# Kernel tuning notes

Measured on AMD Instinct MI355X. Metric: run time of the kernel, lower is better.

The kernel has to match this reference:

```python
import jax, jax.numpy as jnp
import numpy as np

DIM = 2048
N_HEADS = 16
HEAD_DIM = DIM // N_HEADS  # 128
MAX_LEN = 2048
B, T = 2, 2048
RESTORE_SCALE = DIM ** 0.5  # sqkinit / sqkscale = 1 / (1/sqrt(dim))
SQK_SCALE = 1.0 / DIM ** 0.5


def _rope_tables(seq_len, head_dim, dtype=jnp.float32):
    d2 = head_dim // 2
    pos = jnp.arange(seq_len, dtype=dtype)                     # [T]
    theta = 1.0 / (10000.0 ** (jnp.arange(0, head_dim, 2, dtype=dtype) / head_dim))  # [d2]
    ang = pos[:, None] * theta[None, :]                        # [T, d2]
    return jnp.cos(ang), jnp.sin(ang)


def _apply_rope(x, cos, sin):
    # x: [B, H, T, D]; cos/sin: [T, D/2] broadcast over B,H
    d2 = x.shape[-1] // 2
    xr, xi = x[..., :d2], x[..., d2:]
    return jnp.concatenate([xr * cos - xi * sin, xr * sin + xi * cos], axis=-1)


def setup_inputs() -> dict:
    key = jax.random.key(0)
    ks = jax.random.split(key, 5)
    s = 0.02
    return {
        "x":  jax.random.normal(ks[0], (B, T, DIM), jnp.float32),
        "Wq": jax.random.normal(ks[1], (DIM, DIM), jnp.float32) * s,
        "Wk": jax.random.normal(ks[2], (DIM, DIM), jnp.float32) * s,
        "Wv": jax.random.normal(ks[3], (DIM, DIM), jnp.float32) * s,
        "Wo": jax.random.normal(ks[4], (DIM, DIM), jnp.float32) * s,
        "sqk": jnp.ones((N_HEADS, 1, HEAD_DIM), jnp.float32) * SQK_SCALE,
    }


def reference(x, Wq, Wk, Wv, Wo, sqk):
    Bc, Tc, C = x.shape
    # QKV projections (torch Linear: x @ W.T), split heads -> [B, H, T, D]
    def proj(W):
        return (x @ W.T).reshape(Bc, Tc, N_HEADS, HEAD_DIM).transpose(0, 2, 1, 3)
    q, k, v = proj(Wq), proj(Wk), proj(Wv)

    cos, sin = _rope_tables(Tc, HEAD_DIM, x.dtype)
    actual_sqk = sqk * RESTORE_SCALE  # [H, 1, D]
    q = _apply_rope(q, cos, sin) * actual_sqk
    k = _apply_rope(k, cos, sin) * actual_sqk

    # SDPA with scale = sqrt(head_dim) (as in the source, not 1/sqrt)
    scale = HEAD_DIM ** 0.5
    scores = jnp.einsum("bhtd,bhsd->bhts", q, k) * scale  # [B, H, T, T]
    causal = jnp.tril(jnp.ones((Tc, Tc), bool))
    scores = jnp.where(causal, scores, -jnp.inf)
    attn = jax.nn.softmax(scores, axis=-1)
    out = jnp.einsum("bhts,bhsd->bhtd", attn, v)           # [B, H, T, D]
    out = out.transpose(0, 2, 1, 3).reshape(Bc, Tc, C)

    y = out @ Wo.T
    # F.normalize(p=2, dim=-1, eps=1e-12)
    norm = jnp.linalg.norm(y, axis=-1, keepdims=True)
    return y / jnp.maximum(norm, 1e-12)
```

## Files before the change

kernel.cpp:

```cpp
#include <hip/hip_runtime.h>

#define DEVFN __device__ __forceinline__

typedef float    floatx4 __attribute__((ext_vector_type(4)));
typedef _Float16 half8   __attribute__((ext_vector_type(8)));
typedef _Float16 half4v  __attribute__((ext_vector_type(4)));

#define MFMA16H(a, b, c) __builtin_amdgcn_mfma_f32_16x16x32_f16((a), (b), (c), 0, 0, 0)

DEVFN void async16(void* lds, const void* g) {
  __builtin_amdgcn_global_load_lds(
      (const __attribute__((address_space(1))) unsigned int*)g,
      (__attribute__((address_space(3))) unsigned int*)lds, 16, 0, 0);
}
DEVFN half8 ld8h(const _Float16* p) { return *(const half8*)p; }

__global__ __launch_bounds__(256) void cvt_prep(
    const float4* __restrict__ x, const float4* __restrict__ wq,
    const float4* __restrict__ wk, const float4* __restrict__ wv,
    const float4* __restrict__ wo,
    half4v* __restrict__ xh, half4v* __restrict__ xl,
    half4v* __restrict__ qo, half4v* __restrict__ ko,
    half4v* __restrict__ vo, half4v* __restrict__ oo,
    float* __restrict__ cosT, float* __restrict__ sinT) {
  int i = blockIdx.x * 256 + threadIdx.x;
  {
    float4 v = x[i];
    half4v h = {(_Float16)v.x, (_Float16)v.y, (_Float16)v.z, (_Float16)v.w};
    half4v l = {(_Float16)(v.x - (float)h.x), (_Float16)(v.y - (float)h.y),
                (_Float16)(v.z - (float)h.z), (_Float16)(v.w - (float)h.w)};
    xh[i] = h;
    xl[i] = l;
  }
  if (i < 1048576) {
    float4 v = wq[i];
    qo[i] = (half4v){(_Float16)v.x, (_Float16)v.y, (_Float16)v.z, (_Float16)v.w};
    v = wk[i];
    ko[i] = (half4v){(_Float16)v.x, (_Float16)v.y, (_Float16)v.z, (_Float16)v.w};
    v = wv[i];
    vo[i] = (half4v){(_Float16)v.x, (_Float16)v.y, (_Float16)v.z, (_Float16)v.w};
    v = wo[i];
    oo[i] = (half4v){(_Float16)v.x, (_Float16)v.y, (_Float16)v.z, (_Float16)v.w};
  }
  if (i < 131072) {
    int t = i >> 6, d = i & 63;
    double theta = exp(-((double)(2 * d) / 128.0) * log(10000.0));
    double ang = (double)t * theta;
    cosT[i] = (float)cos(ang);
    sinT[i] = (float)sin(ang);
  }
}

__global__ __launch_bounds__(512, 2) void gemm_qk_f16(
    const _Float16* __restrict__ xhp, const _Float16* __restrict__ xlp,
    const _Float16* __restrict__ wqp, const _Float16* __restrict__ wkp,
    const float* __restrict__ cosT, const float* __restrict__ sinT,
    const float* __restrict__ sqk,
    _Float16* __restrict__ qhi, _Float16* __restrict__ qlo,
    _Float16* __restrict__ khi) {
  constexpr int Kd = 2048, NT = 64;
  const int n0 = blockIdx.x * 128, m0 = blockIdx.y * 256;
  const int tid = threadIdx.x, w = tid >> 6, lane = tid & 63;
  const int quad = lane >> 4, l16 = lane & 15;
  const int c0 = w & 1, rb = w >> 1, rgb = rb * 4;
  const int cgr0 = 2 * c0, cgr1 = 2 * c0 + 1, cgr2 = 2 * c0 + 4, cgr3 = 2 * c0 + 5;

  __shared__ __align__(16) _Float16 smem[57344];
  _Float16* XH = smem;
  _Float16* XL = smem + 16384;
  _Float16* WQ = smem + 32768;
  _Float16* WK = smem + 45056;

  floatx4 accQ[4][4], accK[4][4];
#pragma unroll
  for (int i = 0; i < 4; i++)
#pragma unroll
    for (int c = 0; c < 4; c++) {
      accQ[i][c] = (floatx4){0.f, 0.f, 0.f, 0.f};
      accK[i][c] = (floatx4){0.f, 0.f, 0.f, 0.f};
    }

  const size_t xg0 = (size_t)(m0 + 32 * w + l16) * Kd + quad * 8;
  const size_t xg1 = xg0 + (size_t)16 * Kd;
  const size_t wg = (size_t)(n0 + 16 * w + l16) * Kd + quad * 8;

#define STAGE_X(T)                                                      \
  {                                                                     \
    const int kk_ = (T) * 32;                                           \
    _Float16* bx_ = XH + ((T) & 1) * 8192;                              \
    _Float16* bl_ = XL + ((T) & 1) * 8192;                              \
    async16(bx_ + (2 * w) * 512, xhp + xg0 + kk_);                      \
    async16(bx_ + (2 * w + 1) * 512, xhp + xg1 + kk_);                  \
    async16(bl_ + (2 * w) * 512, xlp + xg0 + kk_);                      \
    async16(bl_ + (2 * w + 1) * 512, xlp + xg1 + kk_);                  \
  }
#define STAGE_W(T)                                                      \
  {                                                                     \
    const int kk_ = (T) * 32;                                           \
    async16(WQ + ((T) % 3) * 4096 + w * 512, wqp + wg + kk_);           \
    async16(WK + ((T) % 3) * 4096 + w * 512, wkp + wg + kk_);           \
  }

  STAGE_X(0);
  STAGE_W(0);
  STAGE_W(1);
  asm volatile("s_waitcnt vmcnt(2)" ::: "memory");
  __builtin_amdgcn_s_barrier();

#pragma unroll 1
  for (int t = 0; t < NT; ++t) {
    const _Float16* XH_ = XH + (t & 1) * 8192;
    const _Float16* XL_ = XL + (t & 1) * 8192;
    const _Float16* WQ_ = WQ + (t % 3) * 4096;
    const _Float16* WK_ = WK + (t % 3) * 4096;

    half8 ah[4], al[4], bq[4];
#pragma unroll
    for (int i = 0; i < 4; i++) {
      ah[i] = ld8h(XH_ + (rgb + i) * 512 + lane * 8);
      al[i] = ld8h(XL_ + (rgb + i) * 512 + lane * 8);
    }
    bq[0] = ld8h(WQ_ + cgr0 * 512 + lane * 8);
    bq[1] = ld8h(WQ_ + cgr1 * 512 + lane * 8);
    bq[2] = ld8h(WQ_ + cgr2 * 512 + lane * 8);
    bq[3] = ld8h(WQ_ + cgr3 * 512 + lane * 8);
    if (t + 1 < NT) STAGE_X(t + 1);
    __builtin_amdgcn_s_barrier();
    asm volatile("s_waitcnt lgkmcnt(0)");
    __builtin_amdgcn_sched_barrier(0);
    __builtin_amdgcn_s_setprio(1);
#pragma unroll
    for (int i = 0; i < 4; i++)
#pragma unroll
      for (int c = 0; c < 4; c++)
        accQ[i][c] = MFMA16H(ah[i], bq[c], accQ[i][c]);
#pragma unroll
    for (int i = 0; i < 4; i++)
#pragma unroll
      for (int c = 0; c < 4; c++)
        accQ[i][c] = MFMA16H(al[i], bq[c], accQ[i][c]);
    __builtin_amdgcn_s_setprio(0);
    __builtin_amdgcn_s_barrier();

    half8 bk[4];
    bk[0] = ld8h(WK_ + cgr0 * 512 + lane * 8);
    bk[1] = ld8h(WK_ + cgr1 * 512 + lane * 8);
    bk[2] = ld8h(WK_ + cgr2 * 512 + lane * 8);
    bk[3] = ld8h(WK_ + cgr3 * 512 + lane * 8);
    if (t + 2 < NT) STAGE_W(t + 2);
    __builtin_amdgcn_s_barrier();
    asm volatile("s_waitcnt lgkmcnt(0)");
    __builtin_amdgcn_sched_barrier(0);
    __builtin_amdgcn_s_setprio(1);
#pragma unroll
    for (int i = 0; i < 4; i++)
#pragma unroll
      for (int c = 0; c < 4; c++)
        accK[i][c] = MFMA16H(ah[i], bk[c], accK[i][c]);
#pragma unroll
    for (int i = 0; i < 4; i++)
#pragma unroll
      for (int c = 0; c < 4; c++)
        accK[i][c] = MFMA16H(al[i], bk[c], accK[i][c]);
    __builtin_amdgcn_s_setprio(0);

    if (t + 2 < NT) {
      asm volatile("s_waitcnt vmcnt(2)" ::: "memory");
    } else {
      asm volatile("s_waitcnt vmcnt(0)" ::: "memory");
    }
    __builtin_amdgcn_s_barrier();
  }
#undef STAGE_X
#undef STAGE_W

  _Float16* stH = smem + w * 1152;
  _Float16* stL = smem + 9216 + w * 1152;

  const int h = n0 >> 7;
  const int b = m0 >> 11;

#pragma unroll
  for (int rg = 0; rg < 4; rg++) {
    const int tt0 = (m0 & 2047) + rb * 64 + rg * 16;
    const size_t gbase = (((size_t)(b * 16 + h)) * 2048 + tt0) * 128;

#pragma unroll
    for (int cj = 0; cj < 2; cj++) {
      int d = c0 * 32 + cj * 16 + l16;
      float s1 = sqk[h * 128 + d] * 512.0f;
      float s2 = sqk[h * 128 + d + 64] * 512.0f;
#pragma unroll
      for (int r = 0; r < 4; r++) {
        int tq = tt0 + quad * 4 + r;
        float cc = cosT[tq * 64 + d], sn = sinT[tq * 64 + d];
        float xr = accQ[rg][cj][r], xi = accQ[rg][cj + 2][r];
        float o1 = (xr * cc - xi * sn) * s1;
        float o2 = (xr * sn + xi * cc) * s2;
        _Float16 h1 = (_Float16)o1, h2 = (_Float16)o2;
        int rl = quad * 4 + r;
        stH[rl * 72 + cj * 16 + l16] = h1;
        stH[rl * 72 + 32 + cj * 16 + l16] = h2;
        stL[rl * 72 + cj * 16 + l16] = (_Float16)(o1 - (float)h1);
        stL[rl * 72 + 32 + cj * 16 + l16] = (_Float16)(o2 - (float)h2);
      }
    }
#pragma unroll
    for (int it = 0; it < 2; it++) {
      int row = it * 8 + (lane >> 3), pc = (lane & 7) * 8;
      int d = (pc < 32) ? (c0 * 32 + pc) : (64 + c0 * 32 + (pc - 32));
      size_t ga = gbase + (size_t)row * 128 + d;
      *(half8*)(qhi + ga) = ld8h(&stH[row * 72 + pc]);
      *(half8*)(qlo + ga) = ld8h(&stL[row * 72 + pc]);
    }

#pragma unroll
    for (int cj = 0; cj < 2; cj++) {
      int d = c0 * 32 + cj * 16 + l16;
      float s1 = sqk[h * 128 + d] * 45.254834f;
      float s2 = sqk[h * 128 + d + 64] * 45.254834f;
#pragma unroll
      for (int r = 0; r < 4; r++) {
        int tq = tt0 + quad * 4 + r;
        float cc = cosT[tq * 64 + d], sn = sinT[tq * 64 + d];
        float xr = accK[rg][cj][r], xi = accK[rg][cj + 2][r];
        int rl = quad * 4 + r;
        stH[rl * 72 + cj * 16 + l16] = (_Float16)((xr * cc - xi * sn) * s1);
        stH[rl * 72 + 32 + cj * 16 + l16] = (_Float16)((xr * sn + xi * cc) * s2);
      }
    }
#pragma unroll
    for (int it = 0; it < 2; it++) {
      int row = it * 8 + (lane >> 3), pc = (lane & 7) * 8;
      int d = (pc < 32) ? (c0 * 32 + pc) : (64 + c0 * 32 + (pc - 32));
      *(half8*)(khi + gbase + (size_t)row * 128 + d) = ld8h(&stH[row * 72 + pc]);
    }
  }
}

__global__ __launch_bounds__(512, 2) void gemm_v_f16(
    const _Float16* __restrict__ xhp, const _Float16* __restrict__ wvp,
    _Float16* __restrict__ vt) {
  constexpr int Kd = 2048, NT = 64;
  const int n0 = blockIdx.x * 128, m0 = blockIdx.y * 256;
  const int tid = threadIdx.x, w = tid >> 6, lane = tid & 63;
  const int quad = lane >> 4, l16 = lane & 15;
  const int c0 = w & 1, rb = w >> 1, rgb = rb * 4;

  __shared__ __align__(16) _Float16 smem[28672];
  _Float16* XH = smem;
  _Float16* WV = smem + 16384;

  floatx4 accV[4][4];
#pragma unroll
  for (int i = 0; i < 4; i++)
#pragma unroll
    for (int c = 0; c < 4; c++) accV[i][c] = (floatx4){0.f, 0.f, 0.f, 0.f};

  const size_t xg0 = (size_t)(m0 + 32 * w + l16) * Kd + quad * 8;
  const size_t xg1 = xg0 + (size_t)16 * Kd;
  const size_t wg = (size_t)(n0 + 16 * w + l16) * Kd + quad * 8;

#define STAGE_XV(T)                                                     \
  {                                                                     \
    const int kk_ = (T) * 32;                                           \
    _Float16* bx_ = XH + ((T) & 1) * 8192;                              \
    async16(bx_ + (2 * w) * 512, xhp + xg0 + kk_);                      \
    async16(bx_ + (2 * w + 1) * 512, xhp + xg1 + kk_);                  \
  }
#define STAGE_WV(T)                                                     \
  { async16(WV + ((T) % 3) * 4096 + w * 512, wvp + wg + (T) * 32); }

  STAGE_XV(0);
  STAGE_WV(0);
  STAGE_WV(1);
  asm volatile("s_waitcnt vmcnt(1)" ::: "memory");
  __builtin_amdgcn_s_barrier();

#pragma unroll 1
  for (int t = 0; t < NT; ++t) {
    const _Float16* XH_ = XH + (t & 1) * 8192;
    const _Float16* WV_ = WV + (t % 3) * 4096;

    half8 ah[4], bv[4];
#pragma unroll
    for (int i = 0; i < 4; i++)
      ah[i] = ld8h(XH_ + (rgb + i) * 512 + lane * 8);
#pragma unroll
    for (int c = 0; c < 4; c++)
      bv[c] = ld8h(WV_ + (4 * c0 + c) * 512 + lane * 8);
    if (t + 1 < NT) STAGE_XV(t + 1);
    if (t + 2 < NT) STAGE_WV(t + 2);
    __builtin_amdgcn_s_barrier();
    asm volatile("s_waitcnt lgkmcnt(0)");
    __builtin_amdgcn_sched_barrier(0);
    __builtin_amdgcn_s_setprio(1);
#pragma unroll
    for (int i = 0; i < 4; i++)
#pragma unroll
      for (int c = 0; c < 4; c++)
        accV[i][c] = MFMA16H(ah[i], bv[c], accV[i][c]);
    __builtin_amdgcn_s_setprio(0);
    if (t + 2 < NT) {
      asm volatile("s_waitcnt vmcnt(1)" ::: "memory");
    } else {
      asm volatile("s_waitcnt vmcnt(0)" ::: "memory");
    }
    __builtin_amdgcn_s_barrier();
  }
#undef STAGE_XV
#undef STAGE_WV

  _Float16* stV = smem + w * 1024;

  const int h = n0 >> 7;
  const int b = m0 >> 11;
  const int bh = b * 16 + h;

#pragma unroll
  for (int rg = 0; rg < 4; rg++) {
    const int tt0 = (m0 & 2047) + rb * 64 + rg * 16;
#pragma unroll
    for (int c = 0; c < 4; c++)
#pragma unroll
      for (int r = 0; r < 4; r++)
        stV[(c * 16 + l16) * 16 + quad * 4 + r] = (_Float16)accV[rg][c][r];
#pragma unroll
    for (int it = 0; it < 2; it++) {
      int dl = it * 32 + (lane >> 1), th = (lane & 1) * 8;
      int dh = c0 * 64 + dl;
      size_t ga = ((size_t)bh * 128 + dh) * 2048 + tt0 + th;
      *(half8*)(vt + ga) = ld8h(&stV[dl * 16 + th]);
    }
  }
}

__global__ __launch_bounds__(256, 2) void flash_attn(
    const _Float16* __restrict__ qhp, const _Float16* __restrict__ qlp,
    const _Float16* __restrict__ khp,
    const _Float16* __restrict__ vtp, _Float16* __restrict__ aout) {
  constexpr int T = 2048, HD = 128;
  const int bh = blockIdx.x, qt = blockIdx.y;
  const int q0 = qt * 128;
  const int tid = threadIdx.x, w = tid >> 6, lane = tid & 63;
  const int quad = lane >> 4, l16 = lane & 15;

  __shared__ __align__(16) _Float16 Kh[2][8192];
  __shared__ __align__(16) _Float16 Vt[2][8192];
  __shared__ __align__(16) _Float16 Pb[4][16 * 72];

  const size_t qkbase = (size_t)bh * T * HD;

  half8 qh[2][4], ql[2][4];
#pragma unroll
  for (int i = 0; i < 2; i++)
#pragma unroll
    for (int s = 0; s < 4; s++) {
      size_t off = qkbase + (size_t)(q0 + w * 32 + i * 16 + l16) * HD + s * 32 + quad * 8;
      qh[i][s] = *(const half8*)(qhp + off);
      ql[i][s] = *(const half8*)(qlp + off);
    }

  floatx4 o[2][8];
#pragma unroll
  for (int i = 0; i < 2; i++)
#pragma unroll
    for (int dt = 0; dt < 8; dt++) o[i][dt] = (floatx4){0.f, 0.f, 0.f, 0.f};
  float mrow[2][4], lrow[2][4];
#pragma unroll
  for (int i = 0; i < 2; i++)
#pragma unroll
    for (int r = 0; r < 4; r++) { mrow[i][r] = -3e38f; lrow[i][r] = 0.f; }

  const int ntiles = q0 / 64 + 2;

  auto stageKV = [&](int kt, int set) {
    const int s0 = kt * 64;
    for (int c = w; c < 16; c += 4) {
      int tt = c >> 2, ss = c & 3;
      size_t go = qkbase + (size_t)(s0 + tt * 16 + l16) * HD + ss * 32 + quad * 8;
      async16(&Kh[set][c * 512], khp + go);
      int dt = c >> 1, vs = c & 1;
      size_t vo = (size_t)bh * HD * T + (size_t)(dt * 16 + l16) * T + s0 + vs * 32 + quad * 8;
      async16(&Vt[set][c * 512], vtp + vo);
    }
  };

  stageKV(0, 0);
  __syncthreads();

  for (int kt = 0; kt < ntiles; ++kt) {
    const int s0 = kt * 64;
    const int set = kt & 1;
    if (kt + 1 < ntiles) stageKV(kt + 1, set ^ 1);

    floatx4 S[2][4];
#pragma unroll
    for (int i = 0; i < 2; i++)
#pragma unroll
      for (int j = 0; j < 4; j++) S[i][j] = (floatx4){0.f, 0.f, 0.f, 0.f};

#pragma unroll
    for (int s = 0; s < 4; s++) {
#pragma unroll
      for (int j = 0; j < 4; j++) {
        half8 kh = ld8h(&Kh[set][(j * 4 + s) * 512 + lane * 8]);
        S[0][j] = MFMA16H(qh[0][s], kh, S[0][j]);
        S[1][j] = MFMA16H(qh[1][s], kh, S[1][j]);
        S[0][j] = MFMA16H(ql[0][s], kh, S[0][j]);
        S[1][j] = MFMA16H(ql[1][s], kh, S[1][j]);
      }
    }

    if (s0 + 63 > q0) {
#pragma unroll
      for (int i = 0; i < 2; i++) {
        int rb = q0 + w * 32 + i * 16 + quad * 4;
#pragma unroll
        for (int j = 0; j < 4; j++) {
          int cg = s0 + j * 16 + l16;
#pragma unroll
          for (int r = 0; r < 4; r++)
            if (cg > rb + r) S[i][j][r] = -3e38f;
        }
      }
    }

    half8 pf[2][2];
#pragma unroll
    for (int i = 0; i < 2; i++) {
#pragma unroll
      for (int r = 0; r < 4; r++) {
        float mx = fmaxf(fmaxf(S[i][0][r], S[i][1][r]), fmaxf(S[i][2][r], S[i][3][r]));
#pragma unroll
        for (int d = 1; d < 16; d <<= 1) mx = fmaxf(mx, __shfl_xor(mx, d, 64));
        float mnew = fmaxf(mrow[i][r], mx);
        float al = __expf(mrow[i][r] - mnew);
        mrow[i][r] = mnew;
        float sum = 0.f;
#pragma unroll
        for (int j = 0; j < 4; j++) {
          float p = __expf(S[i][j][r] - mnew);
          S[i][j][r] = p;
          sum += p;
        }
#pragma unroll
        for (int d = 1; d < 16; d <<= 1) sum += __shfl_xor(sum, d, 64);
        lrow[i][r] = lrow[i][r] * al + sum;
#pragma unroll
        for (int dt = 0; dt < 8; dt++) o[i][dt][r] *= al;
      }
#pragma unroll
      for (int r = 0; r < 4; r++)
#pragma unroll
        for (int j = 0; j < 4; j++)
          Pb[w][(quad * 4 + r) * 72 + j * 16 + l16] = (_Float16)S[i][j][r];
      pf[i][0] = ld8h(&Pb[w][l16 * 72 + quad * 8]);
      pf[i][1] = ld8h(&Pb[w][l16 * 72 + 32 + quad * 8]);
    }

#pragma unroll
    for (int dt = 0; dt < 8; dt++) {
#pragma unroll
      for (int s = 0; s < 2; s++) {
        half8 vf = ld8h(&Vt[set][(dt * 2 + s) * 512 + lane * 8]);
        o[0][dt] = MFMA16H(pf[0][s], vf, o[0][dt]);
        o[1][dt] = MFMA16H(pf[1][s], vf, o[1][dt]);
      }
    }
    __syncthreads();
  }

  const int b = bh >> 4, h = bh & 15;
#pragma unroll
  for (int i = 0; i < 2; i++) {
#pragma unroll
    for (int r = 0; r < 4; r++) {
      int trow = q0 + w * 32 + i * 16 + quad * 4 + r;
      float linv = 1.0f / lrow[i][r];
      size_t base = ((size_t)(b * T + trow)) * 2048 + h * 128;
#pragma unroll
      for (int dt = 0; dt < 8; dt++)
        aout[base + dt * 16 + l16] = (_Float16)(o[i][dt][r] * linv);
    }
  }
}

__global__ __launch_bounds__(256, 2) void gemm_o_f16(
    const _Float16* __restrict__ A, const _Float16* __restrict__ B,
    float* __restrict__ outF) {
  constexpr int Kd = 2048;
  constexpr int Nd = 2048;
  const int n0 = blockIdx.x * 128, m0 = blockIdx.y * 128;
  const int tid = threadIdx.x, w = tid >> 6, lane = tid & 63;
  const int quad = lane >> 4, l16 = lane & 15;

  __shared__ __align__(16) _Float16 As[8192];
  __shared__ __align__(16) _Float16 Bs[8192];

  floatx4 acc[2][8];
#pragma unroll
  for (int i = 0; i < 2; i++)
#pragma unroll
    for (int j = 0; j < 8; j++) acc[i][j] = (floatx4){0.f, 0.f, 0.f, 0.f};

  const int t0 = 2 * w, t1 = 2 * w + 1;
  const size_t ao0 = (size_t)(m0 + t0 * 16 + l16) * Kd + quad * 8;
  const size_t ao1 = (size_t)(m0 + t1 * 16 + l16) * Kd + quad * 8;
  const size_t bo0 = (size_t)(n0 + t0 * 16 + l16) * Kd + quad * 8;
  const size_t bo1 = (size_t)(n0 + t1 * 16 + l16) * Kd + quad * 8;

  for (int k0 = 0; k0 < Kd; k0 += 64) {
    __syncthreads();
    async16(&As[t0 * 512], A + ao0 + k0);
    async16(&As[t1 * 512], A + ao1 + k0);
    async16(&As[4096 + t0 * 512], A + ao0 + k0 + 32);
    async16(&As[4096 + t1 * 512], A + ao1 + k0 + 32);
    async16(&Bs[t0 * 512], B + bo0 + k0);
    async16(&Bs[t1 * 512], B + bo1 + k0);
    async16(&Bs[4096 + t0 * 512], B + bo0 + k0 + 32);
    async16(&Bs[4096 + t1 * 512], B + bo1 + k0 + 32);
    __syncthreads();
    half8 a00 = ld8h(&As[t0 * 512 + lane * 8]);
    half8 a10 = ld8h(&As[t1 * 512 + lane * 8]);
    half8 a01 = ld8h(&As[4096 + t0 * 512 + lane * 8]);
    half8 a11 = ld8h(&As[4096 + t1 * 512 + lane * 8]);
#pragma unroll
    for (int j = 0; j < 8; j++) {
      half8 b0 = ld8h(&Bs[j * 512 + lane * 8]);
      acc[0][j] = MFMA16H(a00, b0, acc[0][j]);
      acc[1][j] = MFMA16H(a10, b0, acc[1][j]);
      half8 b1 = ld8h(&Bs[4096 + j * 512 + lane * 8]);
      acc[0][j] = MFMA16H(a01, b1, acc[0][j]);
      acc[1][j] = MFMA16H(a11, b1, acc[1][j]);
    }
  }

#pragma unroll
  for (int i = 0; i < 2; i++) {
    int rbase = m0 + (2 * w + i) * 16 + quad * 4;
#pragma unroll
    for (int j = 0; j < 8; j++) {
      int col = n0 + j * 16 + l16;
#pragma unroll
      for (int r = 0; r < 4; r++)
        outF[(size_t)(rbase + r) * Nd + col] = acc[i][j][r];
    }
  }
}

__global__ __launch_bounds__(256) void rownorm(const float* __restrict__ y,
                                               float* __restrict__ out) {
  int row = blockIdx.x;
  const float4* yr = (const float4*)(y + (size_t)row * 2048);
  float4* od = (float4*)(out + (size_t)row * 2048);
  int t = threadIdx.x;
  float4 v0 = yr[t], v1 = yr[t + 256];
  float ss = v0.x * v0.x + v0.y * v0.y + v0.z * v0.z + v0.w * v0.w +
             v1.x * v1.x + v1.y * v1.y + v1.z * v1.z + v1.w * v1.w;
#pragma unroll
  for (int d = 1; d < 64; d <<= 1) ss += __shfl_xor(ss, d, 64);
  __shared__ float red[4];
  if ((t & 63) == 0) red[t >> 6] = ss;
  __syncthreads();
  float tot = red[0] + red[1] + red[2] + red[3];
  float inv = 1.0f / fmaxf(sqrtf(tot), 1e-12f);
  v0.x *= inv; v0.y *= inv; v0.z *= inv; v0.w *= inv;
  v1.x *= inv; v1.y *= inv; v1.z *= inv; v1.w *= inv;
  od[t] = v0;
  od[t + 256] = v1;
}

extern "C" void kernel_launch(void* const* d_in, const int* in_sizes, int n_in,
                              void* d_out, int out_size, void* d_ws, size_t ws_size,
                              hipStream_t stream) {
  (void)in_sizes; (void)n_in; (void)out_size; (void)ws_size;
  const float* x   = (const float*)d_in[0];
  const float* Wq  = (const float*)d_in[1];
  const float* Wk  = (const float*)d_in[2];
  const float* Wv  = (const float*)d_in[3];
  const float* Wo  = (const float*)d_in[4];
  const float* sqk = (const float*)d_in[5];
  char* ws = (char*)d_ws;

  constexpr size_t SZX = 8388608ull * 2;
  constexpr size_t SZW = 4194304ull * 2;

  size_t o_xh = 0;
  size_t o_xl = o_xh + SZX;
  size_t o_wq = o_xl + SZX;
  size_t o_wk = o_wq + SZW;
  size_t o_wv = o_wk + SZW;
  size_t o_wo = o_wv + SZW;
  size_t o_qh = o_wo + SZW;
  size_t o_ql = o_qh + SZX;
  size_t o_kh = o_ql + SZX;
  size_t o_v  = o_kh + SZX;
  size_t o_vt = o_v + SZX;
  size_t o_cos = o_vt + SZX;
  size_t o_sin = o_cos + 2048 * 64 * 4;
  size_t o_aout = o_wq;
  size_t o_y    = o_qh;

  _Float16* xh = (_Float16*)(ws + o_xh);
  _Float16* xl = (_Float16*)(ws + o_xl);
  _Float16* wq = (_Float16*)(ws + o_wq);
  _Float16* wk = (_Float16*)(ws + o_wk);
  _Float16* wv = (_Float16*)(ws + o_wv);
  _Float16* wo = (_Float16*)(ws + o_wo);
  _Float16* qh = (_Float16*)(ws + o_qh);
  _Float16* ql = (_Float16*)(ws + o_ql);
  _Float16* kh = (_Float16*)(ws + o_kh);
  _Float16* vt = (_Float16*)(ws + o_vt);
  float* cosT = (float*)(ws + o_cos);
  float* sinT = (float*)(ws + o_sin);
  _Float16* aout = (_Float16*)(ws + o_aout);
  float* y = (float*)(ws + o_y);

  cvt_prep<<<8192, 256, 0, stream>>>((const float4*)x, (const float4*)Wq,
                                     (const float4*)Wk, (const float4*)Wv,
                                     (const float4*)Wo, (half4v*)xh, (half4v*)xl,
                                     (half4v*)wq, (half4v*)wk, (half4v*)wv,
                                     (half4v*)wo, cosT, sinT);

  gemm_qk_f16<<<dim3(16, 16), 512, 0, stream>>>(xh, xl, wq, wk, cosT, sinT,
                                                sqk, qh, ql, kh);
  gemm_v_f16<<<dim3(16, 16), 512, 0, stream>>>(xh, wv, vt);

  flash_attn<<<dim3(32, 16), 256, 0, stream>>>(qh, ql, kh, vt, aout);

  gemm_o_f16<<<dim3(16, 32), 256, 0, stream>>>(aout, wo, y);
  rownorm<<<4096, 256, 0, stream>>>(y, (float*)d_out);
}
```

Baseline: 534.3 us.

## Pair causal query tiles per block, add lazy max rescale and MFMA priority

Each flash-attention block now handles two query tiles, p and 15-p, so every block does the same amount of causal work. This halves the grid and removes the load-imbalance tail. The online softmax only rescales the accumulator when some row's new max exceeds the running max by more than 8, which skips most rescales and batches the shuffle reductions across rows. The MFMA sections are wrapped in s_setprio to favour matrix issue; the risks are less parallelism across the grid and larger unnormalized exponents, up to e^8, in fp16 P.

```diff
diff --git a/kernel.cpp b/kernel.cpp
--- a/kernel.cpp
+++ b/kernel.cpp
@@ -340,8 +340,7 @@
     const _Float16* __restrict__ khp,
     const _Float16* __restrict__ vtp, _Float16* __restrict__ aout) {
   constexpr int T = 2048, HD = 128;
-  const int bh = blockIdx.x, qt = blockIdx.y;
-  const int q0 = qt * 128;
+  const int bh = blockIdx.x, p = blockIdx.y;
   const int tid = threadIdx.x, w = tid >> 6, lane = tid & 63;
   const int quad = lane >> 4, l16 = lane & 15;
 
@@ -350,29 +349,7 @@
   __shared__ __align__(16) _Float16 Pb[4][16 * 72];
 
   const size_t qkbase = (size_t)bh * T * HD;
-
-  half8 qh[2][4], ql[2][4];
-#pragma unroll
-  for (int i = 0; i < 2; i++)
-#pragma unroll
-    for (int s = 0; s < 4; s++) {
-      size_t off = qkbase + (size_t)(q0 + w * 32 + i * 16 + l16) * HD + s * 32 + quad * 8;
-      qh[i][s] = *(const half8*)(qhp + off);
-      ql[i][s] = *(const half8*)(qlp + off);
-    }
-
-  floatx4 o[2][8];
-#pragma unroll
-  for (int i = 0; i < 2; i++)
-#pragma unroll
-    for (int dt = 0; dt < 8; dt++) o[i][dt] = (floatx4){0.f, 0.f, 0.f, 0.f};
-  float mrow[2][4], lrow[2][4];
-#pragma unroll
-  for (int i = 0; i < 2; i++)
-#pragma unroll
-    for (int r = 0; r < 4; r++) { mrow[i][r] = -3e38f; lrow[i][r] = 0.f; }
-
-  const int ntiles = q0 / 64 + 2;
+  const size_t vbase = (size_t)bh * HD * T;
 
   auto stageKV = [&](int kt, int set) {
     const int s0 = kt * 64;
@@ -381,107 +358,180 @@
       size_t go = qkbase + (size_t)(s0 + tt * 16 + l16) * HD + ss * 32 + quad * 8;
       async16(&Kh[set][c * 512], khp + go);
       int dt = c >> 1, vs = c & 1;
-      size_t vo = (size_t)bh * HD * T + (size_t)(dt * 16 + l16) * T + s0 + vs * 32 + quad * 8;
+      size_t vo = vbase + (size_t)(dt * 16 + l16) * T + s0 + vs * 32 + quad * 8;
       async16(&Vt[set][c * 512], vtp + vo);
     }
   };
 
-  stageKV(0, 0);
-  __syncthreads();
-
-  for (int kt = 0; kt < ntiles; ++kt) {
-    const int s0 = kt * 64;
-    const int set = kt & 1;
-    if (kt + 1 < ntiles) stageKV(kt + 1, set ^ 1);
-
-    floatx4 S[2][4];
+#pragma unroll 1
+  for (int half = 0; half < 2; ++half) {
+    const int qt = half ? (15 - p) : p;
+    const int q0 = qt * 128;
+
+    half8 qh[2][4], ql[2][4];
 #pragma unroll
     for (int i = 0; i < 2; i++)
 #pragma unroll
-      for (int j = 0; j < 4; j++) S[i][j] = (floatx4){0.f, 0.f, 0.f, 0.f};
-
-#pragma unroll
-    for (int s = 0; s < 4; s++) {
-#pragma unroll
-      for (int j = 0; j < 4; j++) {
-        half8 kh = ld8h(&Kh[set][(j * 4 + s) * 512 + lane * 8]);
-        S[0][j] = MFMA16H(qh[0][s], kh, S[0][j]);
-        S[1][j] = MFMA16H(qh[1][s], kh, S[1][j]);
-        S[0][j] = MFMA16H(ql[0][s], kh, S[0][j]);
-        S[1][j] = MFMA16H(ql[1][s], kh, S[1][j]);
-      }
-    }
-
-    if (s0 + 63 > q0) {
+      for (int s = 0; s < 4; s++) {
+        size_t off = qkbase + (size_t)(q0 + w * 32 + i * 16 + l16) * HD + s * 32 + quad * 8;
+        qh[i][s] = *(const half8*)(qhp + off);
+        ql[i][s] = *(const half8*)(qlp + off);
+      }
+
+    floatx4 o[2][8];
+#pragma unroll
+    for (int i = 0; i < 2; i++)
+#pragma unroll
+      for (int dt = 0; dt < 8; dt++) o[i][dt] = (floatx4){0.f, 0.f, 0.f, 0.f};
+    float mrow[2][4], lrow[2][4];
+#pragma unroll
+    for (int i = 0; i < 2; i++)
+#pragma unroll
+      for (int r = 0; r < 4; r++) { mrow[i][r] = -3e38f; lrow[i][r] = 0.f; }
+
+    const int ntiles = qt * 2 + 2;
+
+    stageKV(0, 0);
+    __syncthreads();
+
+#pragma unroll 1
+    for (int kt = 0; kt < ntiles; ++kt) {
+      const int s0 = kt * 64;
+      const int set = kt & 1;
+      if (kt + 1 < ntiles) stageKV(kt + 1, set ^ 1);
+
+      floatx4 S[2][4];
+#pragma unroll
+      for (int i = 0; i < 2; i++)
+#pragma unroll
+        for (int j = 0; j < 4; j++) S[i][j] = (floatx4){0.f, 0.f, 0.f, 0.f};
+
+      __builtin_amdgcn_s_setprio(1);
+#pragma unroll
+      for (int s = 0; s < 4; s++) {
+#pragma unroll
+        for (int j = 0; j < 4; j++) {
+          half8 kh = ld8h(&Kh[set][(j * 4 + s) * 512 + lane * 8]);
+          S[0][j] = MFMA16H(qh[0][s], kh, S[0][j]);
+          S[1][j] = MFMA16H(qh[1][s], kh, S[1][j]);
+          S[0][j] = MFMA16H(ql[0][s], kh, S[0][j]);
+          S[1][j] = MFMA16H(ql[1][s], kh, S[1][j]);
+        }
+      }
+      __builtin_amdgcn_s_setprio(0);
+
+      if (s0 + 63 > q0) {
+#pragma unroll
+        for (int i = 0; i < 2; i++) {
+          int rb = q0 + w * 32 + i * 16 + quad * 4;
+#pragma unroll
+          for (int j = 0; j < 4; j++) {
+            int cg = s0 + j * 16 + l16;
+#pragma unroll
+            for (int r = 0; r < 4; r++)
+              if (cg > rb + r) S[i][j][r] = -3e38f;
+          }
+        }
+      }
+
+      float lm[2][4];
+#pragma unroll
+      for (int i = 0; i < 2; i++)
+#pragma unroll
+        for (int r = 0; r < 4; r++)
+          lm[i][r] = fmaxf(fmaxf(S[i][0][r], S[i][1][r]),
+                           fmaxf(S[i][2][r], S[i][3][r]));
+
+      bool ok = true;
+#pragma unroll
+      for (int i = 0; i < 2; i++)
+#pragma unroll
+        for (int r = 0; r < 4; r++)
+          ok = ok && (lm[i][r] <= mrow[i][r] + 8.0f);
+
+      if (!__all(ok ? 1 : 0)) {
+#pragma unroll
+        for (int d = 1; d < 16; d <<= 1)
+#pragma unroll
+          for (int i = 0; i < 2; i++)
+#pragma unroll
+            for (int r = 0; r < 4; r++)
+              lm[i][r] = fmaxf(lm[i][r], __shfl_xor(lm[i][r], d, 64));
+#pragma unroll
+        for (int i = 0; i < 2; i++)
+#pragma unroll
+          for (int r = 0; r < 4; r++) {
+            float mnew = fmaxf(mrow[i][r], lm[i][r]);
+            float al = __expf(mrow[i][r] - mnew);
+            mrow[i][r] = mnew;
+            lrow[i][r] *= al;
+#pragma unroll
+            for (int dt = 0; dt < 8; dt++) o[i][dt][r] *= al;
+          }
+      }
+
+      float rs[2][4];
+#pragma unroll
+      for (int i = 0; i < 2; i++)
+#pragma unroll
+        for (int r = 0; r < 4; r++) {
+          float e0 = __expf(S[i][0][r] - mrow[i][r]);
+          float e1 = __expf(S[i][1][r] - mrow[i][r]);
+          float e2 = __expf(S[i][2][r] - mrow[i][r]);
+          float e3 = __expf(S[i][3][r] - mrow[i][r]);
+          S[i][0][r] = e0; S[i][1][r] = e1; S[i][2][r] = e2; S[i][3][r] = e3;
+          rs[i][r] = (e0 + e1) + (e2 + e3);
+        }
+#pragma unroll
+      for (int d = 1; d < 16; d <<= 1)
+#pragma unroll
+        for (int i = 0; i < 2; i++)
+#pragma unroll
+          for (int r = 0; r < 4; r++)
+            rs[i][r] += __shfl_xor(rs[i][r], d, 64);
+#pragma unroll
+      for (int i = 0; i < 2; i++)
+#pragma unroll
+        for (int r = 0; r < 4; r++) lrow[i][r] += rs[i][r];
+
+      half8 pf[2][2];
 #pragma unroll
       for (int i = 0; i < 2; i++) {
-        int rb = q0 + w * 32 + i * 16 + quad * 4;
-#pragma unroll
-        for (int j = 0; j < 4; j++) {
-          int cg = s0 + j * 16 + l16;
-#pragma unroll
-          for (int r = 0; r < 4; r++)
-            if (cg > rb + r) S[i][j][r] = -3e38f;
+#pragma unroll
+        for (int r = 0; r < 4; r++)
+#pragma unroll
+          for (int j = 0; j < 4; j++)
+            Pb[w][(quad * 4 + r) * 72 + j * 16 + l16] = (_Float16)S[i][j][r];
+        pf[i][0] = ld8h(&Pb[w][l16 * 72 + quad * 8]);
+        pf[i][1] = ld8h(&Pb[w][l16 * 72 + 32 + quad * 8]);
+      }
+
+      __builtin_amdgcn_s_setprio(1);
+#pragma unroll
+      for (int dt = 0; dt < 8; dt++) {
+#pragma unroll
+        for (int s = 0; s < 2; s++) {
+          half8 vf = ld8h(&Vt[set][(dt * 2 + s) * 512 + lane * 8]);
+          o[0][dt] = MFMA16H(pf[0][s], vf, o[0][dt]);
+          o[1][dt] = MFMA16H(pf[1][s], vf, o[1][dt]);
         }
       }
-    }
-
-    half8 pf[2][2];
+      __builtin_amdgcn_s_setprio(0);
+      __syncthreads();
+    }
+
+    const int b = bh >> 4, h = bh & 15;
 #pragma unroll
     for (int i = 0; i < 2; i++) {
 #pragma unroll
       for (int r = 0; r < 4; r++) {
-        float mx = fmaxf(fmaxf(S[i][0][r], S[i][1][r]), fmaxf(S[i][2][r], S[i][3][r]));
-#pragma unroll
-        for (int d = 1; d < 16; d <<= 1) mx = fmaxf(mx, __shfl_xor(mx, d, 64));
-        float mnew = fmaxf(mrow[i][r], mx);
-        float al = __expf(mrow[i][r] - mnew);
-        mrow[i][r] = mnew;
-        float sum = 0.f;
-#pragma unroll
-        for (int j = 0; j < 4; j++) {
-          float p = __expf(S[i][j][r] - mnew);
-          S[i][j][r] = p;
-          sum += p;
-        }
-#pragma unroll
-        for (int d = 1; d < 16; d <<= 1) sum += __shfl_xor(sum, d, 64);
-        lrow[i][r] = lrow[i][r] * al + sum;
-#pragma unroll
-        for (int dt = 0; dt < 8; dt++) o[i][dt][r] *= al;
-      }
-#pragma unroll
-      for (int r = 0; r < 4; r++)
-#pragma unroll
-        for (int j = 0; j < 4; j++)
-          Pb[w][(quad * 4 + r) * 72 + j * 16 + l16] = (_Float16)S[i][j][r];
-      pf[i][0] = ld8h(&Pb[w][l16 * 72 + quad * 8]);
-      pf[i][1] = ld8h(&Pb[w][l16 * 72 + 32 + quad * 8]);
-    }
-
-#pragma unroll
-    for (int dt = 0; dt < 8; dt++) {
-#pragma unroll
-      for (int s = 0; s < 2; s++) {
-        half8 vf = ld8h(&Vt[set][(dt * 2 + s) * 512 + lane * 8]);
-        o[0][dt] = MFMA16H(pf[0][s], vf, o[0][dt]);
-        o[1][dt] = MFMA16H(pf[1][s], vf, o[1][dt]);
-      }
-    }
-    __syncthreads();
-  }
-
-  const int b = bh >> 4, h = bh & 15;
-#pragma unroll
-  for (int i = 0; i < 2; i++) {
-#pragma unroll
-    for (int r = 0; r < 4; r++) {
-      int trow = q0 + w * 32 + i * 16 + quad * 4 + r;
-      float linv = 1.0f / lrow[i][r];
-      size_t base = ((size_t)(b * T + trow)) * 2048 + h * 128;
-#pragma unroll
-      for (int dt = 0; dt < 8; dt++)
-        aout[base + dt * 16 + l16] = (_Float16)(o[i][dt][r] * linv);
+        int trow = q0 + w * 32 + i * 16 + quad * 4 + r;
+        float linv = 1.0f / lrow[i][r];
+        size_t base = ((size_t)(b * T + trow)) * 2048 + h * 128;
+#pragma unroll
+        for (int dt = 0; dt < 8; dt++)
+          aout[base + dt * 16 + l16] = (_Float16)(o[i][dt][r] * linv);
+      }
     }
   }
 }
@@ -627,7 +677,7 @@
                                                 sqk, qh, ql, kh);
   gemm_v_f16<<<dim3(16, 16), 512, 0, stream>>>(xh, wv, vt);
 
-  flash_attn<<<dim3(32, 16), 256, 0, stream>>>(qh, ql, kh, vt, aout);
+  flash_attn<<<dim3(32, 8), 256, 0, stream>>>(qh, ql, kh, vt, aout);
 
   gemm_o_f16<<<dim3(16, 32), 256, 0, stream>>>(aout, wo, y);
   rownorm<<<4096, 256, 0, stream>>>(y, (float*)d_out);
```

Measured after the change: 527.6 us. Within noise of the previous version (-1.3%).

## Halve flash-attention query tile, reverse tile order, add lazy rescale and setprio

Applied to the files above, without the earlier changes.

The flash attention kernel now gives each block 64 query rows instead of 128, so each wave owns 16 rows, and the grid doubles to 32x32. Query tiles are scheduled longest-first by reversing the block index. The online softmax skips the max reduction and rescale when every lane's new local max stays within 8 of the running max. MFMA sections are wrapped in s_setprio. The aim is better occupancy, load balance across causal tiles and less softmax overhead, at the cost of more K/V reloads per query row and larger unnormalised exponent ranges in fp16 P.

```diff
diff --git a/kernel.cpp b/kernel.cpp
--- a/kernel.cpp
+++ b/kernel.cpp
@@ -340,8 +340,9 @@
     const _Float16* __restrict__ khp,
     const _Float16* __restrict__ vtp, _Float16* __restrict__ aout) {
   constexpr int T = 2048, HD = 128;
-  const int bh = blockIdx.x, qt = blockIdx.y;
-  const int q0 = qt * 128;
+  const int bh = blockIdx.x;
+  const int qt = 31 - blockIdx.y;
+  const int q0 = qt * 64;
   const int tid = threadIdx.x, w = tid >> 6, lane = tid & 63;
   const int quad = lane >> 4, l16 = lane & 15;
 
@@ -350,29 +351,7 @@
   __shared__ __align__(16) _Float16 Pb[4][16 * 72];
 
   const size_t qkbase = (size_t)bh * T * HD;
-
-  half8 qh[2][4], ql[2][4];
-#pragma unroll
-  for (int i = 0; i < 2; i++)
-#pragma unroll
-    for (int s = 0; s < 4; s++) {
-      size_t off = qkbase + (size_t)(q0 + w * 32 + i * 16 + l16) * HD + s * 32 + quad * 8;
-      qh[i][s] = *(const half8*)(qhp + off);
-      ql[i][s] = *(const half8*)(qlp + off);
-    }
-
-  floatx4 o[2][8];
-#pragma unroll
-  for (int i = 0; i < 2; i++)
-#pragma unroll
-    for (int dt = 0; dt < 8; dt++) o[i][dt] = (floatx4){0.f, 0.f, 0.f, 0.f};
-  float mrow[2][4], lrow[2][4];
-#pragma unroll
-  for (int i = 0; i < 2; i++)
-#pragma unroll
-    for (int r = 0; r < 4; r++) { mrow[i][r] = -3e38f; lrow[i][r] = 0.f; }
-
-  const int ntiles = q0 / 64 + 2;
+  const size_t vbase = (size_t)bh * HD * T;
 
   auto stageKV = [&](int kt, int set) {
     const int s0 = kt * 64;
@@ -381,108 +360,138 @@
       size_t go = qkbase + (size_t)(s0 + tt * 16 + l16) * HD + ss * 32 + quad * 8;
       async16(&Kh[set][c * 512], khp + go);
       int dt = c >> 1, vs = c & 1;
-      size_t vo = (size_t)bh * HD * T + (size_t)(dt * 16 + l16) * T + s0 + vs * 32 + quad * 8;
+      size_t vo = vbase + (size_t)(dt * 16 + l16) * T + s0 + vs * 32 + quad * 8;
       async16(&Vt[set][c * 512], vtp + vo);
     }
   };
+
+  half8 qh[4], ql[4];
+#pragma unroll
+  for (int s = 0; s < 4; s++) {
+    size_t off = qkbase + (size_t)(q0 + w * 16 + l16) * HD + s * 32 + quad * 8;
+    qh[s] = *(const half8*)(qhp + off);
+    ql[s] = *(const half8*)(qlp + off);
+  }
+
+  floatx4 o[8];
+#pragma unroll
+  for (int dt = 0; dt < 8; dt++) o[dt] = (floatx4){0.f, 0.f, 0.f, 0.f};
+  float mrow[4], lrow[4];
+#pragma unroll
+  for (int r = 0; r < 4; r++) { mrow[r] = -3e38f; lrow[r] = 0.f; }
+
+  const int ntiles = qt + 1;
 
   stageKV(0, 0);
   __syncthreads();
 
+#pragma unroll 1
   for (int kt = 0; kt < ntiles; ++kt) {
     const int s0 = kt * 64;
     const int set = kt & 1;
     if (kt + 1 < ntiles) stageKV(kt + 1, set ^ 1);
 
-    floatx4 S[2][4];
-#pragma unroll
-    for (int i = 0; i < 2; i++)
-#pragma unroll
-      for (int j = 0; j < 4; j++) S[i][j] = (floatx4){0.f, 0.f, 0.f, 0.f};
-
+    floatx4 S[4];
+#pragma unroll
+    for (int j = 0; j < 4; j++) S[j] = (floatx4){0.f, 0.f, 0.f, 0.f};
+
+    __builtin_amdgcn_s_setprio(1);
 #pragma unroll
     for (int s = 0; s < 4; s++) {
 #pragma unroll
       for (int j = 0; j < 4; j++) {
         half8 kh = ld8h(&Kh[set][(j * 4 + s) * 512 + lane * 8]);
-        S[0][j] = MFMA16H(qh[0][s], kh, S[0][j]);
-        S[1][j] = MFMA16H(qh[1][s], kh, S[1][j]);
-        S[0][j] = MFMA16H(ql[0][s], kh, S[0][j]);
-        S[1][j] = MFMA16H(ql[1][s], kh, S[1][j]);
+        S[j] = MFMA16H(qh[s], kh, S[j]);
+        S[j] = MFMA16H(ql[s], kh, S[j]);
       }
     }
-
-    if (s0 + 63 > q0) {
-#pragma unroll
-      for (int i = 0; i < 2; i++) {
-        int rb = q0 + w * 32 + i * 16 + quad * 4;
-#pragma unroll
-        for (int j = 0; j < 4; j++) {
-          int cg = s0 + j * 16 + l16;
-#pragma unroll
-          for (int r = 0; r < 4; r++)
-            if (cg > rb + r) S[i][j][r] = -3e38f;
-        }
+    __builtin_amdgcn_s_setprio(0);
+
+    if (kt == ntiles - 1) {
+      int rbase = q0 + w * 16 + quad * 4;
+#pragma unroll
+      for (int j = 0; j < 4; j++) {
+        int cg = s0 + j * 16 + l16;
+#pragma unroll
+        for (int r = 0; r < 4; r++)
+          if (cg > rbase + r) S[j][r] = -3e38f;
       }
     }
 
-    half8 pf[2][2];
-#pragma unroll
-    for (int i = 0; i < 2; i++) {
+    float lm[4];
+#pragma unroll
+    for (int r = 0; r < 4; r++)
+      lm[r] = fmaxf(fmaxf(S[0][r], S[1][r]), fmaxf(S[2][r], S[3][r]));
+
+    bool ok = true;
+#pragma unroll
+    for (int r = 0; r < 4; r++) ok = ok && (lm[r] <= mrow[r] + 8.0f);
+
+    if (!__all(ok ? 1 : 0)) {
+#pragma unroll
+      for (int d = 1; d < 16; d <<= 1)
+#pragma unroll
+        for (int r = 0; r < 4; r++)
+          lm[r] = fmaxf(lm[r], __shfl_xor(lm[r], d, 64));
 #pragma unroll
       for (int r = 0; r < 4; r++) {
-        float mx = fmaxf(fmaxf(S[i][0][r], S[i][1][r]), fmaxf(S[i][2][r], S[i][3][r]));
-#pragma unroll
-        for (int d = 1; d < 16; d <<= 1) mx = fmaxf(mx, __shfl_xor(mx, d, 64));
-        float mnew = fmaxf(mrow[i][r], mx);
-        float al = __expf(mrow[i][r] - mnew);
-        mrow[i][r] = mnew;
-        float sum = 0.f;
-#pragma unroll
-        for (int j = 0; j < 4; j++) {
-          float p = __expf(S[i][j][r] - mnew);
-          S[i][j][r] = p;
-          sum += p;
-        }
-#pragma unroll
-        for (int d = 1; d < 16; d <<= 1) sum += __shfl_xor(sum, d, 64);
-        lrow[i][r] = lrow[i][r] * al + sum;
-#pragma unroll
-        for (int dt = 0; dt < 8; dt++) o[i][dt][r] *= al;
+        float mnew = fmaxf(mrow[r], lm[r]);
+        float al = __expf(mrow[r] - mnew);
+        mrow[r] = mnew;
+        lrow[r] *= al;
+#pragma unroll
+        for (int dt = 0; dt < 8; dt++) o[dt][r] *= al;
       }
-#pragma unroll
-      for (int r = 0; r < 4; r++)
-#pragma unroll
-        for (int j = 0; j < 4; j++)
-          Pb[w][(quad * 4 + r) * 72 + j * 16 + l16] = (_Float16)S[i][j][r];
-      pf[i][0] = ld8h(&Pb[w][l16 * 72 + quad * 8]);
-      pf[i][1] = ld8h(&Pb[w][l16 * 72 + 32 + quad * 8]);
-    }
-
+    }
+
+    float rs[4];
+#pragma unroll
+    for (int r = 0; r < 4; r++) {
+      float e0 = __expf(S[0][r] - mrow[r]);
+      float e1 = __expf(S[1][r] - mrow[r]);
+      float e2 = __expf(S[2][r] - mrow[r]);
+      float e3 = __expf(S[3][r] - mrow[r]);
+      S[0][r] = e0; S[1][r] = e1; S[2][r] = e2; S[3][r] = e3;
+      rs[r] = (e0 + e1) + (e2 + e3);
+    }
+#pragma unroll
+    for (int d = 1; d < 16; d <<= 1)
+#pragma unroll
+      for (int r = 0; r < 4; r++) rs[r] += __shfl_xor(rs[r], d, 64);
+#pragma unroll
+    for (int r = 0; r < 4; r++) lrow[r] += rs[r];
+
+    half8 pf[2];
+#pragma unroll
+    for (int r = 0; r < 4; r++)
+#pragma unroll
+      for (int j = 0; j < 4; j++)
+        Pb[w][(quad * 4 + r) * 72 + j * 16 + l16] = (_Float16)S[j][r];
+    pf[0] = ld8h(&Pb[w][l16 * 72 + quad * 8]);
+    pf[1] = ld8h(&Pb[w][l16 * 72 + 32 + quad * 8]);
+
+    __builtin_amdgcn_s_setprio(1);
 #pragma unroll
     for (int dt = 0; dt < 8; dt++) {
 #pragma unroll
       for (int s = 0; s < 2; s++) {
         half8 vf = ld8h(&Vt[set][(dt * 2 + s) * 512 + lane * 8]);
-        o[0][dt] = MFMA16H(pf[0][s], vf, o[0][dt]);
-        o[1][dt] = MFMA16H(pf[1][s], vf, o[1][dt]);
+        o[dt] = MFMA16H(pf[s], vf, o[dt]);
       }
     }
+    __builtin_amdgcn_s_setprio(0);
     __syncthreads();
   }
 
   const int b = bh >> 4, h = bh & 15;
 #pragma unroll
-  for (int i = 0; i < 2; i++) {
-#pragma unroll
-    for (int r = 0; r < 4; r++) {
-      int trow = q0 + w * 32 + i * 16 + quad * 4 + r;
-      float linv = 1.0f / lrow[i][r];
-      size_t base = ((size_t)(b * T + trow)) * 2048 + h * 128;
-#pragma unroll
-      for (int dt = 0; dt < 8; dt++)
-        aout[base + dt * 16 + l16] = (_Float16)(o[i][dt][r] * linv);
-    }
+  for (int r = 0; r < 4; r++) {
+    int trow = q0 + w * 16 + quad * 4 + r;
+    float linv = 1.0f / lrow[r];
+    size_t base = ((size_t)(b * T + trow)) * 2048 + h * 128;
+#pragma unroll
+    for (int dt = 0; dt < 8; dt++)
+      aout[base + dt * 16 + l16] = (_Float16)(o[dt][r] * linv);
   }
 }
 
@@ -627,7 +636,7 @@
                                                 sqk, qh, ql, kh);
   gemm_v_f16<<<dim3(16, 16), 512, 0, stream>>>(xh, wv, vt);
 
-  flash_attn<<<dim3(32, 16), 256, 0, stream>>>(qh, ql, kh, vt, aout);
+  flash_attn<<<dim3(32, 32), 256, 0, stream>>>(qh, ql, kh, vt, aout);
 
   gemm_o_f16<<<dim3(16, 32), 256, 0, stream>>>(aout, wo, y);
   rownorm<<<4096, 256, 0, stream>>>(y, (float*)d_out);
```

Result: faster. 496.5 us (-7.1%).
